# Kernel tuning notes

Hardware: AMD Instinct MI355X
Metric: run time of the kernel (lower is better)

Reference implementation:

```python
import jax, jax.numpy as jnp
import numpy as np

B, T, I, H, L, O = 32, 2048, 256, 512, 2, 256


def _cell(xg, h, c, Whh, bhh):
    # xg: precomputed/current input-to-hidden projection incl. b_ih, shape [B, 4H]
    gates = xg + h @ Whh.T + bhh
    i, f, g, o = jnp.split(gates, 4, axis=-1)
    i = jax.nn.sigmoid(i)
    f = jax.nn.sigmoid(f)
    g = jnp.tanh(g)
    o = jax.nn.sigmoid(o)
    c2 = f * c + i * g
    h2 = o * jnp.tanh(c2)
    return h2, c2


def setup_inputs() -> dict:
    key = jax.random.key(0)
    ks = jax.random.split(key, 11)
    s_i = 1.0 / np.sqrt(H)
    return {
        "x": jax.random.normal(ks[0], (B, T, I), jnp.float32),
        "W_ih0": jax.random.normal(ks[1], (4 * H, I), jnp.float32) * s_i,
        "W_hh0": jax.random.normal(ks[2], (4 * H, H), jnp.float32) * s_i,
        "b_ih0": jax.random.normal(ks[3], (4 * H,), jnp.float32) * s_i,
        "b_hh0": jax.random.normal(ks[4], (4 * H,), jnp.float32) * s_i,
        "W_ih1": jax.random.normal(ks[5], (4 * H, H), jnp.float32) * s_i,
        "W_hh1": jax.random.normal(ks[6], (4 * H, H), jnp.float32) * s_i,
        "b_ih1": jax.random.normal(ks[7], (4 * H,), jnp.float32) * s_i,
        "b_hh1": jax.random.normal(ks[8], (4 * H,), jnp.float32) * s_i,
        "fc_w": jax.random.normal(ks[9], (O, H), jnp.float32) * s_i,
        "fc_b": jax.random.normal(ks[10], (O,), jnp.float32) * s_i,
    }


def reference(x, W_ih0, W_hh0, b_ih0, b_hh0, W_ih1, W_hh1, b_ih1, b_hh1, fc_w, fc_b):
    # Precompute layer-0 input projections for all timesteps in one big GEMM.
    xproj = jnp.einsum('bti,gi->tbg', x, W_ih0) + b_ih0  # [T, B, 4H]

    h0 = jnp.zeros((x.shape[0], H), x.dtype)
    carry0 = (h0, h0, h0, h0)  # (h_l0, c_l0, h_l1, c_l1)

    def step(carry, xg_t):
        h_0, c_0, h_1, c_1 = carry
        h_0, c_0 = _cell(xg_t, h_0, c_0, W_hh0, b_hh0)
        xg1 = h_0 @ W_ih1.T + b_ih1
        h_1, c_1 = _cell(xg1, h_1, c_1, W_hh1, b_hh1)
        return (h_0, c_0, h_1, c_1), None

    (h_0, c_0, h_1, c_1), _ = jax.lax.scan(step, carry0, xproj)
    # Original takes last timestep's top-layer hidden, then fc.
    return h_1 @ fc_w.T + fc_b
```

## Files before the change

### kernel.cpp

```cpp
#include <hip/hip_runtime.h>
#include <hip/hip_bf16.h>

typedef __hip_bfloat16 bf16;
typedef unsigned long long u64;
typedef unsigned int u32;
typedef unsigned short u16;
using short8 = __attribute__((ext_vector_type(8))) short;
using f32x4  = __attribute__((ext_vector_type(4))) float;

#define T_STEPS 2048
#define IDIM    256
#define HDIM    512
#define NBLK    128
#define R0      8
#define HWW     8192
#define LROW    528
#define TAGMASK 0x0000ffff0000ffffULL

__device__ __forceinline__ float sigm(float x) { return 1.0f / (1.0f + __expf(-x)); }
__device__ __forceinline__ float tanh_f(float x) {
  x = fminf(fmaxf(x, -15.f), 15.f);
  float e = __expf(2.f * x);
  return (e - 1.f) / (e + 1.f);
}
__device__ __forceinline__ u16 bfbits(float f) {
  bf16 b = __float2bfloat16(f); u16 s; __builtin_memcpy(&s, &b, 2); return s;
}
__device__ __forceinline__ short8 cvt8(const float* __restrict__ p) {
  float4 lo = *(const float4*)(const void*)p;
  float4 hi = *(const float4*)(const void*)(p + 4);
  short8 r;
  r[0] = (short)bfbits(lo.x); r[1] = (short)bfbits(lo.y); r[2] = (short)bfbits(lo.z); r[3] = (short)bfbits(lo.w);
  r[4] = (short)bfbits(hi.x); r[5] = (short)bfbits(hi.y); r[6] = (short)bfbits(hi.z); r[7] = (short)bfbits(hi.w);
  return r;
}

__device__ __forceinline__ u64 ldg8(const u64* p) {
  return __hip_atomic_load(p, __ATOMIC_RELAXED, __HIP_MEMORY_SCOPE_AGENT);
}
__device__ __forceinline__ u32 ldg4(const u32* p) {
  return __hip_atomic_load(p, __ATOMIC_RELAXED, __HIP_MEMORY_SCOPE_AGENT);
}
__device__ __forceinline__ void stg4(u32* p, u32 v) {
  __hip_atomic_store(p, v, __ATOMIC_RELAXED, __HIP_MEMORY_SCOPE_AGENT);
}

__device__ __forceinline__ int wave_min_i(int v) {
#pragma unroll
  for (int off = 32; off > 0; off >>= 1) {
    int o = __shfl_xor(v, off, 64);
    v = v < o ? v : o;
  }
  return v;
}

__device__ __forceinline__ void probe_wait(const u32* __restrict__ slot, u32 tag, int lane) {
  const u32* p0 = slot + lane * 8;
  for (;;) {
    u32 a = ldg4(p0);
    u32 b = ldg4(p0 + 4);
    if (__all(((a & 0xffffu) == tag) && ((b & 0xffffu) == tag))) return;
  }
}

__device__ __forceinline__ void ldsw(bf16* dst, int i, int tid, u64 v) {
  u32 lo = (u32)v, hi = (u32)(v >> 32);
  *(u32*)(void*)(dst + i * LROW + tid * 2) = (lo >> 16) | (hi & 0xffff0000u);
}

__device__ __forceinline__ void gather(const u32* __restrict__ src, bf16* dst,
                                       int tid, u32 tag) {
  const u64* s = (const u64*)(const void*)src;
  const u64 tt = ((u64)tag << 32) | tag;
  u64 v[16];
#pragma unroll
  for (int i = 0; i < 16; i++) v[i] = ldg8(s + tid + i * 256);
  unsigned bad = 0xffffu;
  while (bad) {
    unsigned nb = 0;
#pragma unroll
    for (int i = 0; i < 16; i++)
      if (bad & (1u << i)) {
        if ((v[i] & TAGMASK) != tt) { v[i] = ldg8(s + tid + i * 256); nb |= 1u << i; }
      }
    bad = nb;
  }
#pragma unroll
  for (int i = 0; i < 16; i++) ldsw(dst, i, tid, v[i]);
}

#define MFMA(a, b, c) __builtin_amdgcn_mfma_f32_16x16x32_bf16((a), (b), (c), 0, 0, 0)

__global__ void __launch_bounds__(256, 1) lstm_probe2p(
    const float* __restrict__ x,
    const float* __restrict__ Wih0, const float* __restrict__ Whh0,
    const float* __restrict__ bih0, const float* __restrict__ bhh0,
    const float* __restrict__ Wih1, const float* __restrict__ Whh1,
    const float* __restrict__ bih1, const float* __restrict__ bhh1,
    const float* __restrict__ fcw, const float* __restrict__ fcb,
    float* __restrict__ out,
    u32* __restrict__ ring0g,
    u32* __restrict__ ring1g) {
  __shared__ __align__(16) bf16 lds_h0[16 * LROW];
  __shared__ __align__(16) bf16 lds_h1[16 * LROW];

  const int tid  = threadIdx.x;
  const int w    = tid >> 6, lane = tid & 63;
  const int q    = lane >> 4, m = lane & 15, q8 = q * 8;
  const int bx   = (int)blockIdx.x;
  const int g    = bx >> 6;
  const int rr   = bx & 63;
  const bool l0  = (rr < 32);
  const int blk  = rr & 31;
  const int jb   = blk * 16 + w * 4;
  const int unit = jb + (m >> 2), gate = m & 3;
  const int wrow = gate * HDIM + unit;
  const int ju   = jb + q;
  const f32x4 zero = {0.f, 0.f, 0.f, 0.f};

  u32* ring0 = ring0g + (size_t)g * R0 * HWW;
  u32* ring1 = ring1g + (size_t)g * 2 * HWW;

  short8 A[32];
  f32x4 bias;
  if (l0) {
#pragma unroll
    for (int kc = 0; kc < 8; kc++)  A[kc]      = cvt8(Wih0 + wrow * IDIM + kc * 32 + q8);
#pragma unroll
    for (int kc = 0; kc < 16; kc++) A[8 + kc]  = cvt8(Whh0 + wrow * HDIM + kc * 32 + q8);
#pragma unroll
    for (int r = 0; r < 4; r++)
      bias[r] = bih0[r * HDIM + ju] + bhh0[r * HDIM + ju];
  } else {
#pragma unroll
    for (int kc = 0; kc < 16; kc++) A[kc]      = cvt8(Wih1 + wrow * HDIM + kc * 32 + q8);
#pragma unroll
    for (int kc = 0; kc < 16; kc++) A[16 + kc] = cvt8(Whh1 + wrow * HDIM + kc * 32 + q8);
#pragma unroll
    for (int r = 0; r < 4; r++)
      bias[r] = bih1[r * HDIM + ju] + bhh1[r * HDIM + ju];
  }

  float c_a = 0.f;

  if (l0) {
    f32x4 an0 = bias;
    {
      const float* xa = x + (size_t)(g * 16 + m) * (T_STEPS * IDIM) + q8;
#pragma unroll
      for (int kc = 0; kc < 8; kc++) an0 = MFMA(A[kc], cvt8(xa + kc * 32), an0);
    }
    int est = R0 - 1;
    for (int p = 0; p < T_STEPS; ++p) {
      f32x4 a0 = an0;
      if (p > 0) {
        probe_wait(ring0 + ((p - 1) & (R0 - 1)) * HWW, (u32)p, lane);
        gather(ring0 + ((p - 1) & (R0 - 1)) * HWW, lds_h0, tid, (u32)p);
        __syncthreads();
        f32x4 b0 = zero;
#pragma unroll
        for (int kc = 0; kc < 8; kc++) {
          short8 r0 = *(const short8*)(const void*)(lds_h0 + m * LROW + kc * 32 + q8);
          a0 = MFMA(A[8 + kc], r0, a0);
          short8 s0 = *(const short8*)(const void*)(lds_h0 + m * LROW + (kc + 8) * 32 + q8);
          b0 = MFMA(A[16 + kc], s0, b0);
        }
        a0 = a0 + b0;
      }
      float ia = sigm(a0[0]), fa = sigm(a0[1]), ga = tanh_f(a0[2]), oa = sigm(a0[3]);
      c_a = fa * c_a + ia * ga;
      u32 word = ((u32)bfbits(oa * tanh_f(c_a)) << 16) | (u32)(p + 1);

      if (p >= R0 && est < p) {
        int mn;
        do {
          u32 sw = ldg4(ring1 + (p & 1) * HWW + (lane & 31) * 16);
          mn = wave_min_i((int)(short)(sw & 0xffffu));
        } while (mn < p - (R0 - 1));
        est = mn + (R0 - 1);
      }
      stg4(ring0 + (p & (R0 - 1)) * HWW + (m << 9) + ju, word);

      if (p + 1 < T_STEPS) {
        an0 = bias;
        const float* xa = x + (size_t)(g * 16 + m) * (T_STEPS * IDIM)
                        + (size_t)(p + 1) * IDIM + q8;
#pragma unroll
        for (int kc = 0; kc < 8; kc++) an0 = MFMA(A[kc], cvt8(xa + kc * 32), an0);
      }
      __syncthreads();
    }

    if (blk < 16) {
      probe_wait(ring1 + ((T_STEPS - 1) & 1) * HWW, (u32)T_STEPS, lane);
      gather(ring1 + ((T_STEPS - 1) & 1) * HWW, lds_h0, tid, (u32)T_STEPS);
      __syncthreads();
      if (w == 0) {
        const int obase = blk * 16;
        f32x4 a0;
#pragma unroll
        for (int r = 0; r < 4; r++) a0[r] = fcb[obase + 4 * q + r];
        const float* Ar = fcw + (size_t)(obase + m) * HDIM + q8;
#pragma unroll
        for (int kc = 0; kc < 16; kc++) {
          short8 af = cvt8(Ar + kc * 32);
          short8 b0 = *(const short8*)(const void*)(lds_h0 + m * LROW + kc * 32 + q8);
          a0 = MFMA(af, b0, a0);
        }
#pragma unroll
        for (int r = 0; r < 4; r++)
          out[(size_t)(g * 16 + m) * 256 + obase + 4 * q + r] = a0[r];
      }
    }
  } else {
    for (int p = 0; p < T_STEPS; ++p) {
      probe_wait(ring0 + (p & (R0 - 1)) * HWW, (u32)(p + 1), lane);
      gather(ring0 + (p & (R0 - 1)) * HWW, lds_h0, tid, (u32)(p + 1));
      __syncthreads();

      f32x4 c0 = bias, c1 = zero, c2 = zero, c3 = zero;
#pragma unroll
      for (int kc = 0; kc < 8; kc++) {
        short8 r0 = *(const short8*)(const void*)(lds_h0 + m * LROW + kc * 32 + q8);
        c0 = MFMA(A[kc], r0, c0);
        short8 s0 = *(const short8*)(const void*)(lds_h0 + m * LROW + (kc + 8) * 32 + q8);
        c1 = MFMA(A[8 + kc], s0, c1);
      }
      if (p > 0) {
        probe_wait(ring1 + ((p - 1) & 1) * HWW, (u32)p, lane);
        gather(ring1 + ((p - 1) & 1) * HWW, lds_h1, tid, (u32)p);
        __syncthreads();
#pragma unroll
        for (int kc = 0; kc < 8; kc++) {
          short8 r0 = *(const short8*)(const void*)(lds_h1 + m * LROW + kc * 32 + q8);
          c2 = MFMA(A[16 + kc], r0, c2);
          short8 s0 = *(const short8*)(const void*)(lds_h1 + m * LROW + (kc + 8) * 32 + q8);
          c3 = MFMA(A[24 + kc], s0, c3);
        }
      }
      f32x4 a0 = (c0 + c1) + (c2 + c3);
      float ia = sigm(a0[0]), fa = sigm(a0[1]), ga = tanh_f(a0[2]), oa = sigm(a0[3]);
      c_a = fa * c_a + ia * ga;
      u32 word = ((u32)bfbits(oa * tanh_f(c_a)) << 16) | (u32)(p + 1);
      stg4(ring1 + (p & 1) * HWW + (m << 9) + ju, word);
      if (p == 0) __syncthreads();
    }
  }
}

extern "C" void kernel_launch(void* const* d_in, const int* in_sizes, int n_in,
                              void* d_out, int out_size, void* d_ws, size_t ws_size,
                              hipStream_t stream) {
  const float* x    = (const float*)d_in[0];
  const float* Wih0 = (const float*)d_in[1];
  const float* Whh0 = (const float*)d_in[2];
  const float* bih0 = (const float*)d_in[3];
  const float* bhh0 = (const float*)d_in[4];
  const float* Wih1 = (const float*)d_in[5];
  const float* Whh1 = (const float*)d_in[6];
  const float* bih1 = (const float*)d_in[7];
  const float* bhh1 = (const float*)d_in[8];
  const float* fcw  = (const float*)d_in[9];
  const float* fcb  = (const float*)d_in[10];

  u32* ring0g = (u32*)d_ws;
  u32* ring1g = (u32*)((char*)d_ws + (size_t)2 * R0 * HWW * sizeof(u32));

  hipLaunchKernelGGL(lstm_probe2p, dim3(NBLK), dim3(256), 0, stream,
                     x, Wih0, Whh0, bih0, bhh0, Wih1, Whh1, bih1, bhh1, fcw, fcb,
                     (float*)d_out, ring0g, ring1g);
}
```

Baseline: 8.855 ms.

## Overlap layer-1 ring gathers and drop redundant block barriers

The layer-1 blocks now issue the global loads for both the layer-0 hidden-state ring and the layer-1 recurrent ring before validating either, then fill LDS with one barrier per step instead of two. The separate layer-0 probe wait is dropped, since the tag check in the validation loop already spins until the data is current. The trailing per-step barrier in the layer-0 loop and the one-off step-0 barrier in layer 1 are also removed. This shortens the serial latency chain on each recurrent step. It relies on the tag-based ring waits to keep LDS buffers from being overwritten while slower waves still read them, and it spins on a full 16-load refetch rather than a light probe.

```diff
diff --git a/kernel.cpp b/kernel.cpp
--- a/kernel.cpp
+++ b/kernel.cpp
@@ -68,13 +68,9 @@
   *(u32*)(void*)(dst + i * LROW + tid * 2) = (lo >> 16) | (hi & 0xffff0000u);
 }
 
-__device__ __forceinline__ void gather(const u32* __restrict__ src, bf16* dst,
-                                       int tid, u32 tag) {
-  const u64* s = (const u64*)(const void*)src;
+__device__ __forceinline__ void validate_ldsw(const u64* __restrict__ s, u64* v,
+                                              bf16* dst, int tid, u32 tag) {
   const u64 tt = ((u64)tag << 32) | tag;
-  u64 v[16];
-#pragma unroll
-  for (int i = 0; i < 16; i++) v[i] = ldg8(s + tid + i * 256);
   unsigned bad = 0xffffu;
   while (bad) {
     unsigned nb = 0;
@@ -89,9 +85,18 @@
   for (int i = 0; i < 16; i++) ldsw(dst, i, tid, v[i]);
 }
 
+__device__ __forceinline__ void gather1(const u32* __restrict__ src, bf16* dst,
+                                        int tid, u32 tag) {
+  const u64* s = (const u64*)(const void*)src;
+  u64 v[16];
+#pragma unroll
+  for (int i = 0; i < 16; i++) v[i] = ldg8(s + tid + i * 256);
+  validate_ldsw(s, v, dst, tid, tag);
+}
+
 #define MFMA(a, b, c) __builtin_amdgcn_mfma_f32_16x16x32_bf16((a), (b), (c), 0, 0, 0)
 
-__global__ void __launch_bounds__(256, 1) lstm_probe2p(
+__global__ void __launch_bounds__(256, 1) lstm_ovl2p(
     const float* __restrict__ x,
     const float* __restrict__ Wih0, const float* __restrict__ Whh0,
     const float* __restrict__ bih0, const float* __restrict__ bhh0,
@@ -155,7 +160,7 @@
       f32x4 a0 = an0;
       if (p > 0) {
         probe_wait(ring0 + ((p - 1) & (R0 - 1)) * HWW, (u32)p, lane);
-        gather(ring0 + ((p - 1) & (R0 - 1)) * HWW, lds_h0, tid, (u32)p);
+        gather1(ring0 + ((p - 1) & (R0 - 1)) * HWW, lds_h0, tid, (u32)p);
         __syncthreads();
         f32x4 b0 = zero;
 #pragma unroll
@@ -188,12 +193,11 @@
 #pragma unroll
         for (int kc = 0; kc < 8; kc++) an0 = MFMA(A[kc], cvt8(xa + kc * 32), an0);
       }
-      __syncthreads();
     }
 
     if (blk < 16) {
       probe_wait(ring1 + ((T_STEPS - 1) & 1) * HWW, (u32)T_STEPS, lane);
-      gather(ring1 + ((T_STEPS - 1) & 1) * HWW, lds_h0, tid, (u32)T_STEPS);
+      gather1(ring1 + ((T_STEPS - 1) & 1) * HWW, lds_h0, tid, (u32)T_STEPS);
       __syncthreads();
       if (w == 0) {
         const int obase = blk * 16;
@@ -214,8 +218,20 @@
     }
   } else {
     for (int p = 0; p < T_STEPS; ++p) {
-      probe_wait(ring0 + (p & (R0 - 1)) * HWW, (u32)(p + 1), lane);
-      gather(ring0 + (p & (R0 - 1)) * HWW, lds_h0, tid, (u32)(p + 1));
+      const u64* s0 = (const u64*)(const void*)(ring0 + (p & (R0 - 1)) * HWW);
+      u64 v0[16];
+#pragma unroll
+      for (int i = 0; i < 16; i++) v0[i] = ldg8(s0 + tid + i * 256);
+
+      const u64* s1 = (const u64*)(const void*)(ring1 + ((p - 1) & 1) * HWW);
+      u64 v1[16];
+      if (p > 0) {
+        probe_wait(ring1 + ((p - 1) & 1) * HWW, (u32)p, lane);
+#pragma unroll
+        for (int i = 0; i < 16; i++) v1[i] = ldg8(s1 + tid + i * 256);
+      }
+      validate_ldsw(s0, v0, lds_h0, tid, (u32)(p + 1));
+      if (p > 0) validate_ldsw(s1, v1, lds_h1, tid, (u32)p);
       __syncthreads();
 
       f32x4 c0 = bias, c1 = zero, c2 = zero, c3 = zero;
@@ -223,19 +239,16 @@
       for (int kc = 0; kc < 8; kc++) {
         short8 r0 = *(const short8*)(const void*)(lds_h0 + m * LROW + kc * 32 + q8);
         c0 = MFMA(A[kc], r0, c0);
-        short8 s0 = *(const short8*)(const void*)(lds_h0 + m * LROW + (kc + 8) * 32 + q8);
-        c1 = MFMA(A[8 + kc], s0, c1);
+        short8 s0f = *(const short8*)(const void*)(lds_h0 + m * LROW + (kc + 8) * 32 + q8);
+        c1 = MFMA(A[8 + kc], s0f, c1);
       }
       if (p > 0) {
-        probe_wait(ring1 + ((p - 1) & 1) * HWW, (u32)p, lane);
-        gather(ring1 + ((p - 1) & 1) * HWW, lds_h1, tid, (u32)p);
-        __syncthreads();
 #pragma unroll
         for (int kc = 0; kc < 8; kc++) {
           short8 r0 = *(const short8*)(const void*)(lds_h1 + m * LROW + kc * 32 + q8);
           c2 = MFMA(A[16 + kc], r0, c2);
-          short8 s0 = *(const short8*)(const void*)(lds_h1 + m * LROW + (kc + 8) * 32 + q8);
-          c3 = MFMA(A[24 + kc], s0, c3);
+          short8 s0f = *(const short8*)(const void*)(lds_h1 + m * LROW + (kc + 8) * 32 + q8);
+          c3 = MFMA(A[24 + kc], s0f, c3);
         }
       }
       f32x4 a0 = (c0 + c1) + (c2 + c3);
@@ -243,7 +256,6 @@
       c_a = fa * c_a + ia * ga;
       u32 word = ((u32)bfbits(oa * tanh_f(c_a)) << 16) | (u32)(p + 1);
       stg4(ring1 + (p & 1) * HWW + (m << 9) + ju, word);
-      if (p == 0) __syncthreads();
     }
   }
 }
@@ -266,7 +278,7 @@
   u32* ring0g = (u32*)d_ws;
   u32* ring1g = (u32*)((char*)d_ws + (size_t)2 * R0 * HWW * sizeof(u32));
 
-  hipLaunchKernelGGL(lstm_probe2p, dim3(NBLK), dim3(256), 0, stream,
+  hipLaunchKernelGGL(lstm_ovl2p, dim3(NBLK), dim3(256), 0, stream,
                      x, Wih0, Whh0, bih0, bhh0, Wih1, Whh1, bih1, bhh1, fcw, fcb,
                      (float*)d_out, ring0g, ring1g);
 }
```

Measured after the change: 8.696 ms. No clear change (-1.8%).
